# Kernel optimization log

Measured on AMD Instinct MI355X. Metric: run time of the kernel, lower is better.

## Reference

```python
import jax, jax.numpy as jnp
import numpy as np
import math

DIM = 768
EMB = 768          # dim * num_heads (num_heads=1)
NBLOCKS = 4
M = EMB // 2       # kernel_ratio = 0.5 -> 384 random features
EPS = 1e-8


def monarch_linear(x, w1, w2, b):
    """Monarch (blockdiag butterfly) linear: x [..., n] -> [..., out].
    w1: (k, q, p) with n = k*p ; w2: (l, s, r) with k*q = l*r ; out = l*s."""
    lead = x.shape[:-1]
    k, q, p = w1.shape
    l, s, r = w2.shape
    xf = x.reshape(-1, k, p)                              # (B, k, p)
    o1 = jnp.einsum('bkp,kqp->bkq', xf, w1)               # (B, k, q)
    o1 = o1.transpose(0, 2, 1).reshape(-1, l, r)          # permute then (B, l, r)
    o2 = jnp.einsum('blr,lsr->bls', o1, w2)               # (B, l, s)
    out = o2.transpose(0, 2, 1).reshape(*lead, s * l)     # (B, s, l) flattened
    return out + b


def prm_exp(x, w):
    """FAVOR+ positive random features. x: [b,t,d], w: [m,d]."""
    xd = 0.5 * jnp.sum(x * x, axis=-1, keepdims=True)     # [b,t,1]
    wtx = jnp.einsum('btd,md->btm', x, w)                 # [b,t,m]
    return jnp.exp(wtx - xd) / math.sqrt(M)


def _monarch_params(rng, n_in, n_out, nblocks):
    in_blk = n_in // nblocks
    out_blk = n_out // nblocks
    if n_in < n_out:
        w1 = rng.standard_normal((nblocks, in_blk, in_blk)).astype(np.float32)
        w2 = rng.standard_normal((nblocks, out_blk, in_blk)).astype(np.float32)
    else:
        w1 = rng.standard_normal((nblocks, out_blk, in_blk)).astype(np.float32)
        w2 = rng.standard_normal((nblocks, out_blk, out_blk)).astype(np.float32)
    scale = 1.0 / math.sqrt(n_in)
    b = rng.standard_normal((n_out,)).astype(np.float32) * scale
    return w1 * scale, w2 * scale, b


def setup_inputs() -> dict:
    key = jax.random.key(0)
    x = jax.random.normal(key, (8, 4096, DIM), dtype=jnp.float32)
    rng = np.random.default_rng(0)
    kqv_w1, kqv_w2, kqv_b = _monarch_params(rng, DIM, 3 * EMB, NBLOCKS)
    proj_w1, proj_w2, proj_b = _monarch_params(rng, EMB, EMB, NBLOCKS)
    # orthogonal random-feature matrix, rows orthonormal, scaled by sqrt(m)
    a = rng.standard_normal((EMB, M)).astype(np.float64)
    qmat, _ = np.linalg.qr(a)                             # (EMB, M), cols orthonormal
    w = (qmat.T * math.sqrt(M)).astype(np.float32)        # (M, EMB)
    return {
        'x': x,
        'kqv_w1': jnp.asarray(kqv_w1), 'kqv_w2': jnp.asarray(kqv_w2), 'kqv_b': jnp.asarray(kqv_b),
        'proj_w1': jnp.asarray(proj_w1), 'proj_w2': jnp.asarray(proj_w2), 'proj_b': jnp.asarray(proj_b),
        'w': jnp.asarray(w),
    }


def reference(x, kqv_w1, kqv_w2, kqv_b, proj_w1, proj_w2, proj_b, w):
    kqv = monarch_linear(x, kqv_w1, kqv_w2, kqv_b)        # [b,t,3*EMB]
    k, q, v = jnp.split(kqv, 3, axis=-1)                  # order k,q,v as in torch.split
    kp = prm_exp(k, w)                                    # [b,t,m]
    qp = prm_exp(q, w)                                    # [b,t,m]
    D = jnp.einsum('btm,bm->bt', qp, kp.sum(axis=1))[:, :, None]   # [b,t,1]
    kptv = jnp.einsum('btn,btm->bnm', v, kp)              # [b,EMB,m]
    y = jnp.einsum('btm,bnm->btn', qp, kptv) / (D + EPS)  # [b,t,EMB]
    return monarch_linear(y, proj_w1, proj_w2, proj_b)
```

## Files before the change

kernel.cpp:

```cpp
#include <hip/hip_runtime.h>


#define NTOK   32768
#define RSQRTM 0.05103103630798288f

typedef _Float16 f16;
typedef f16   f16x8 __attribute__((ext_vector_type(8)));
typedef f16   f16x4 __attribute__((ext_vector_type(4)));
typedef f16   f16x2 __attribute__((ext_vector_type(2)));
typedef short s16x8 __attribute__((ext_vector_type(8)));
typedef float f32x4 __attribute__((ext_vector_type(4)));

typedef const void __attribute__((address_space(1))) gv_t;
typedef void       __attribute__((address_space(3))) lv_t;
#define GLL16(g, l) __builtin_amdgcn_global_load_lds((gv_t*)(g), (lv_t*)(l), 16, 0, 0)

__device__ __forceinline__ float b2f(unsigned short u){
  union{unsigned int i; float f;} v; v.i = ((unsigned int)u)<<16; return v.f;
}
__device__ __forceinline__ unsigned short f2b(float f){
  union{float f; unsigned int i;} v; v.f = f;
  unsigned int x = v.i;
  x += 0x7fffu + ((x>>16)&1u);
  return (unsigned short)(x>>16);
}

template<typename T> struct MfmaOp;
template<> struct MfmaOp<f16> {
  typedef f16x8 frag;
  static __device__ __forceinline__ f32x4 run(frag a, frag b, f32x4 c){
    return __builtin_amdgcn_mfma_f32_16x16x32_f16(a, b, c, 0, 0, 0);
  }
};
template<> struct MfmaOp<short> {
  typedef s16x8 frag;
  static __device__ __forceinline__ f32x4 run(frag a, frag b, f32x4 c){
    return __builtin_amdgcn_mfma_f32_16x16x32_bf16(a, b, c, 0, 0, 0);
  }
};

__global__ void cvt16(const float4* __restrict__ src, f16* __restrict__ dst, int n4){
  const int i = blockIdx.x*256 + threadIdx.x;
  if (i >= n4) return;
  const float4 v = src[i];
  f16x4 h; h[0]=(f16)v.x; h[1]=(f16)v.y; h[2]=(f16)v.z; h[3]=(f16)v.w;
  *reinterpret_cast<f16x4*>(dst + 4*(long)i) = h;
}
__global__ void build_wkqvT(const float* __restrict__ w1, const float* __restrict__ w2,
                            f16* __restrict__ Wt){
  const int idx = blockIdx.x*256 + threadIdx.x;
  const int j = idx / 768, i = idx % 768;
  const int k = i / 192, p = i % 192;
  const int s = j >> 2,  l = j & 3;
  float acc = 0.f;
  #pragma unroll 4
  for(int u=0; u<48; ++u)
    acc += w1[(k*192 + l*48+u)*192 + p] * w2[(l*576+s)*192 + 4*u+k];
  Wt[idx] = (f16)acc;
}
__global__ void build_wprojT(const float* __restrict__ w1, const float* __restrict__ w2,
                             unsigned short* __restrict__ Wt){
  const int idx = blockIdx.x*256 + threadIdx.x;
  const int j = idx / 768, i = idx % 768;
  const int k = i / 192, p = i % 192;
  const int s = j >> 2,  l = j & 3;
  float acc = 0.f;
  #pragma unroll 4
  for(int u=0; u<48; ++u)
    acc += w1[(k*192 + l*48+u)*192 + p] * w2[(l*192+s)*192 + 4*u+k];
  Wt[idx] = f2b(acc);
}

template<typename T, int BM, int BN, int EPI>
__global__ __launch_bounds__(256)
void mgemm(const T* __restrict__ A, int lda, long aB,
           const T* __restrict__ Bt, int ldb, long bB,
           int K, void* __restrict__ out, int ldo, long outB,
           void* __restrict__ out2,
           const float* __restrict__ aux, long auxB){
  constexpr int MT = BM/32, NT = BN/32;
  constexpr int IA = BM/64, IB = BN/64;
  __shared__ T As[BM*32];
  __shared__ T Bs[BN*32];
  typedef typename MfmaOp<T>::frag frag_t;

  const int tid = threadIdx.x, lane = tid & 63, w = tid >> 6;
  const int wm = w >> 1, wn = w & 1;
  const int bz = blockIdx.z;
  const long m0 = (long)blockIdx.y * BM;
  const int  n0 = blockIdx.x * BN;
  const T* Ab = A  + (long)bz*aB;
  const T* Bb = Bt + (long)bz*bB;

  f32x4 acc[MT][NT];
  const f32x4 zero = {0.f, 0.f, 0.f, 0.f};
  #pragma unroll
  for(int i=0;i<MT;i++)
    #pragma unroll
    for(int j=0;j<NT;j++) acc[i][j] = zero;

  for (int k0 = 0; k0 < K; k0 += 32){
    __syncthreads();
    #pragma unroll
    for (int i = 0; i < IA; ++i){
      const int e = (w*IA + i)*64 + lane;
      const int m = e >> 2, j = e & 3;
      GLL16(Ab + (m0 + m)*lda + k0 + j*8, As + (size_t)(w*IA + i)*512);
    }
    #pragma unroll
    for (int i = 0; i < IB; ++i){
      const int e = (w*IB + i)*64 + lane;
      const int n = e >> 2, j = e & 3;
      GLL16(Bb + (long)(n0 + n)*ldb + k0 + j*8, Bs + (size_t)(w*IB + i)*512);
    }
    __syncthreads();

    frag_t a[MT], b[NT];
    #pragma unroll
    for (int mt=0; mt<MT; ++mt)
      a[mt] = *reinterpret_cast<const frag_t*>(
        &As[(wm*MT*16 + mt*16 + (lane&15))*32 + (lane>>4)*8]);
    #pragma unroll
    for (int nt=0; nt<NT; ++nt)
      b[nt] = *reinterpret_cast<const frag_t*>(
        &Bs[(wn*NT*16 + nt*16 + (lane&15))*32 + (lane>>4)*8]);
    #pragma unroll
    for (int mt=0; mt<MT; ++mt)
      #pragma unroll
      for (int nt=0; nt<NT; ++nt)
        acc[mt][nt] = MfmaOp<T>::run(a[mt], b[nt], acc[mt][nt]);
  }

  const int q = lane >> 4, ln = lane & 15;
  #pragma unroll
  for (int mt=0; mt<MT; ++mt){
    const long mbase = m0 + wm*MT*16 + mt*16 + q*4;
    float xv[4];
    if constexpr(EPI==1 || EPI==2){
      #pragma unroll
      for(int r=0;r<4;r++) xv[r] = aux[mbase + r];
    }
    if constexpr(EPI==4){
      #pragma unroll
      for(int r=0;r<4;r++) xv[r] = 1.f/(aux[bz*auxB + mbase + r] + 1e-8f);
    }
    #pragma unroll
    for (int nt=0; nt<NT; ++nt){
      const int n = n0 + wn*NT*16 + nt*16 + ln;
      const f32x4 c = acc[mt][nt];
      if constexpr(EPI==0){
        if (n0 < 1536){
          f16* KQ = (f16*)out;
          const float bv = aux[n];
          #pragma unroll
          for(int r=0;r<4;r++) KQ[(mbase+r)*1536 + n] = (f16)(c[r] + bv);
        } else {
          unsigned short* VT = (unsigned short*)out2;
          const float bv = aux[n];
          ushort4 v;
          v.x = f2b(c[0]+bv); v.y = f2b(c[1]+bv); v.z = f2b(c[2]+bv); v.w = f2b(c[3]+bv);
          *reinterpret_cast<ushort4*>(&VT[(long)(n-1536)*32768 + mbase]) = v;
        }
      } else if constexpr(EPI==1){
        unsigned short* o = (unsigned short*)out;
        ushort4 v;
        v.x = f2b(__expf(c[0]-xv[0])*RSQRTM);
        v.y = f2b(__expf(c[1]-xv[1])*RSQRTM);
        v.z = f2b(__expf(c[2]-xv[2])*RSQRTM);
        v.w = f2b(__expf(c[3]-xv[3])*RSQRTM);
        *reinterpret_cast<ushort4*>(&o[(long)n*ldo + mbase]) = v;
      } else if constexpr(EPI==2){
        unsigned short* o = (unsigned short*)out;
        #pragma unroll
        for(int r=0;r<4;r++)
          o[(mbase+r)*ldo + n] = f2b(__expf(c[r]-xv[r])*RSQRTM);
      } else if constexpr(EPI==3){
        unsigned short* o = (unsigned short*)out + (long)bz*outB;
        #pragma unroll
        for(int r=0;r<4;r++) o[(mbase+r)*ldo + n] = f2b(c[r]);
      } else if constexpr(EPI==4){
        unsigned short* o = (unsigned short*)out + (long)bz*outB;
        #pragma unroll
        for(int r=0;r<4;r++) o[(mbase+r)*ldo + n] = f2b(c[r]*xv[r]);
      } else {
        float* o = (float*)out;
        const float bv = aux[n];
        #pragma unroll
        for(int r=0;r<4;r++) o[(mbase+r)*ldo + n] = c[r] + bv;
      }
    }
  }
}

__global__ void xd_kernel(const f16* __restrict__ KQ, float* __restrict__ xd){
  const int t = blockIdx.x*4 + (threadIdx.x>>6);
  const int lane = threadIdx.x & 63;
  const f16* row = KQ + (long)t*1536;
  float sk=0.f, sq=0.f;
  #pragma unroll
  for(int j=0;j<6;j++){
    const f16x2 a = *reinterpret_cast<const f16x2*>(&row[lane*2 + j*128]);
    const f16x2 b = *reinterpret_cast<const f16x2*>(&row[768 + lane*2 + j*128]);
    const float a0=(float)a[0], a1=(float)a[1], b0=(float)b[0], b1=(float)b[1];
    sk += a0*a0 + a1*a1;  sq += b0*b0 + b1*b1;
  }
  for(int off=32; off; off>>=1){ sk += __shfl_down(sk,off); sq += __shfl_down(sq,off); }
  if(lane==0){ xd[t] = 0.5f*sk; xd[NTOK + t] = 0.5f*sq; }
}
__global__ void ksum_kernel(const unsigned short* __restrict__ kpT, float* __restrict__ ksum){
  const int lane = threadIdx.x & 63, w = threadIdx.x >> 6;
  const int id = blockIdx.x*4 + w;
  const int m = id % 384, b = id / 384;
  const unsigned short* base = kpT + (long)m*32768 + b*4096;
  float acc = 0.f;
  #pragma unroll
  for(int j=0;j<16;j++){
    const ushort4 v = *reinterpret_cast<const ushort4*>(&base[lane*4 + j*256]);
    acc += b2f(v.x)+b2f(v.y)+b2f(v.z)+b2f(v.w);
  }
  for(int off=32; off; off>>=1) acc += __shfl_down(acc,off);
  if(lane==0) ksum[id] = acc;
}
__global__ void d_kernel(const unsigned short* __restrict__ qp,
                         const float* __restrict__ ksum, float* __restrict__ Dv){
  const int t = blockIdx.x*4 + (threadIdx.x>>6);
  const int lane = threadIdx.x & 63;
  const int b = t >> 12;
  const unsigned short* row = qp + (long)t*384;
  const float* ks = ksum + b*384;
  float acc = 0.f;
  #pragma unroll
  for(int j=0;j<6;j++){ const int m = lane + 64*j; acc += b2f(row[m])*ks[m]; }
  for(int off=32; off; off>>=1) acc += __shfl_down(acc,off);
  if(lane==0) Dv[t] = acc;
}

extern "C" void kernel_launch(void* const* d_in, const int* in_sizes, int n_in,
                              void* d_out, int out_size, void* d_ws, size_t ws_size,
                              hipStream_t stream){
  const float* x       = (const float*)d_in[0];
  const float* kqv_w1  = (const float*)d_in[1];
  const float* kqv_w2  = (const float*)d_in[2];
  const float* kqv_b   = (const float*)d_in[3];
  const float* proj_w1 = (const float*)d_in[4];
  const float* proj_w2 = (const float*)d_in[5];
  const float* proj_b  = (const float*)d_in[6];
  const float* w       = (const float*)d_in[7];
  char* ws = (char*)d_ws;

  const size_t o_WkqvT  = 0;
  const size_t o_WprojT = 3538944;
  const size_t o_w16    = 4718592;
  const size_t o_x16    = 5308416;
  const size_t o_KQ     = 55640064;
  const size_t o_VT     = 156303360;
  const size_t o_xd     = 206635008;
  const size_t o_kpT    = 206897152;
  const size_t o_qp     = 232062976;
  const size_t o_ksum   = 257228800;
  const size_t o_kptv   = 257241088;
  const size_t o_Dv     = 261959680;
  const size_t o_Y      = 262090752;
  const size_t TOTAL    = 312422400;
  if (ws_size < TOTAL) return;

  f16*            WkqvT  = (f16*)(ws + o_WkqvT);
  short*          WprojT = (short*)(ws + o_WprojT);
  f16*            w16    = (f16*)(ws + o_w16);
  f16*            x16    = (f16*)(ws + o_x16);
  f16*            KQ     = (f16*)(ws + o_KQ);
  short*          VT     = (short*)(ws + o_VT);
  float*          xd     = (float*)(ws + o_xd);
  short*          kpT    = (short*)(ws + o_kpT);
  short*          qp     = (short*)(ws + o_qp);
  float*          ksum   = (float*)(ws + o_ksum);
  short*          kptv   = (short*)(ws + o_kptv);
  float*          Dv     = (float*)(ws + o_Dv);
  short*          Y      = (short*)(ws + o_Y);

  cvt16<<<24576, 256, 0, stream>>>((const float4*)x, x16, 6291456);
  cvt16<<<288,   256, 0, stream>>>((const float4*)w, w16, 73728);
  build_wkqvT <<<6912, 256, 0, stream>>>(kqv_w1, kqv_w2, WkqvT);
  build_wprojT<<<2304, 256, 0, stream>>>(proj_w1, proj_w2, (unsigned short*)WprojT);

  mgemm<f16,128,128,0><<<dim3(18,256,1), 256, 0, stream>>>(
      x16, 768, 0L, WkqvT, 768, 0L, 768, KQ, 1536, 0L, VT, kqv_b, 0L);
  xd_kernel<<<8192, 256, 0, stream>>>(KQ, xd);

  mgemm<f16,128,128,1><<<dim3(3,256,1), 256, 0, stream>>>(
      KQ, 1536, 0L, w16, 768, 0L, 768, kpT, 32768, 0L, nullptr, xd, 0L);
  mgemm<f16,128,128,2><<<dim3(3,256,1), 256, 0, stream>>>(
      KQ + 768, 1536, 0L, w16, 768, 0L, 768, qp, 384, 0L, nullptr, xd + NTOK, 0L);

  ksum_kernel<<<768, 256, 0, stream>>>((const unsigned short*)kpT, ksum);

  mgemm<short,64,64,3><<<dim3(6,12,8), 256, 0, stream>>>(
      VT, 32768, 4096L, kpT, 32768, 4096L, 4096, kptv, 384, 294912L, nullptr, nullptr, 0L);

  d_kernel<<<8192, 256, 0, stream>>>((const unsigned short*)qp, ksum, Dv);

  mgemm<short,128,128,4><<<dim3(6,32,8), 256, 0, stream>>>(
      qp, 384, 1572864L, kptv, 384, 294912L, 384, Y, 768, 3145728L, nullptr, Dv, 4096L);

  mgemm<short,128,128,5><<<dim3(6,256,1), 256, 0, stream>>>(
      Y, 768, 0L, WprojT, 768, 0L, 768, d_out, 768, 0L, nullptr, proj_b, 0L);
}
```

Measured before the change: 678.8 us.

## Fuse reductions into GEMM epilogues, deepen K tile with swizzled LDS, split-K kptv

Folds the xd, ksum and D reductions into the GEMM epilogues using shuffles and atomics, removing three standalone reduction kernels and their re-reads of KQ, kpT and qp. The GEMM K step doubles to 64 with an XOR-swizzled LDS layout to cut LDS bank conflicts and halve the barrier count. The kptv GEMM becomes a 4-way split-K with 128x128 tiles writing fp32 partials, followed by a reduce kernel, which raises parallelism for that long-K GEMM. This adds atomics, a memset, extra workspace and fp32 partial traffic, and LDS use per block doubles.

```diff
diff --git a/kernel.cpp b/kernel.cpp
--- a/kernel.cpp
+++ b/kernel.cpp
@@ -7,7 +7,6 @@
 typedef _Float16 f16;
 typedef f16   f16x8 __attribute__((ext_vector_type(8)));
 typedef f16   f16x4 __attribute__((ext_vector_type(4)));
-typedef f16   f16x2 __attribute__((ext_vector_type(2)));
 typedef short s16x8 __attribute__((ext_vector_type(8)));
 typedef float f32x4 __attribute__((ext_vector_type(4)));
 
@@ -70,27 +69,37 @@
     acc += w1[(k*192 + l*48+u)*192 + p] * w2[(l*192+s)*192 + 4*u+k];
   Wt[idx] = f2b(acc);
 }
-
-template<typename T, int BM, int BN, int EPI>
+__global__ void reduce_kptv(const float* __restrict__ p32, unsigned short* __restrict__ o){
+  const int idx = blockIdx.x*256 + threadIdx.x;
+  const int b = idx / 294912, i = idx % 294912;
+  const float* base = p32 + (long)b*4*294912 + i;
+  o[idx] = f2b(base[0] + base[294912] + base[2*294912] + base[3*294912]);
+}
+
+template<typename T, int BM, int BN, int EPI, int SPLIT>
 __global__ __launch_bounds__(256)
 void mgemm(const T* __restrict__ A, int lda, long aB,
            const T* __restrict__ Bt, int ldb, long bB,
            int K, void* __restrict__ out, int ldo, long outB,
            void* __restrict__ out2,
-           const float* __restrict__ aux, long auxB){
+           const float* __restrict__ aux, long auxB,
+           float* __restrict__ aux2){
   constexpr int MT = BM/32, NT = BN/32;
-  constexpr int IA = BM/64, IB = BN/64;
-  __shared__ T As[BM*32];
-  __shared__ T Bs[BN*32];
+  constexpr int IA = BM/32, IB = BN/32;
+  __shared__ T As[BM*64];
+  __shared__ T Bs[BN*64];
   typedef typename MfmaOp<T>::frag frag_t;
 
   const int tid = threadIdx.x, lane = tid & 63, w = tid >> 6;
   const int wm = w >> 1, wn = w & 1;
+  const int ln = lane & 15, q = lane >> 4;
   const int bz = blockIdx.z;
+  const int batch = bz / SPLIT;
+  const int kstart = (bz % SPLIT) * K;
   const long m0 = (long)blockIdx.y * BM;
   const int  n0 = blockIdx.x * BN;
-  const T* Ab = A  + (long)bz*aB;
-  const T* Bb = Bt + (long)bz*bB;
+  const T* Ab = A  + (long)batch*aB;
+  const T* Bb = Bt + (long)batch*bB;
 
   f32x4 acc[MT][NT];
   const f32x4 zero = {0.f, 0.f, 0.f, 0.f};
@@ -99,145 +108,183 @@
     #pragma unroll
     for(int j=0;j<NT;j++) acc[i][j] = zero;
 
-  for (int k0 = 0; k0 < K; k0 += 32){
+  for (int k0 = kstart; k0 < kstart + K; k0 += 64){
     __syncthreads();
     #pragma unroll
     for (int i = 0; i < IA; ++i){
       const int e = (w*IA + i)*64 + lane;
-      const int m = e >> 2, j = e & 3;
+      const int m = e >> 3, j = (e & 7) ^ (m & 7);
       GLL16(Ab + (m0 + m)*lda + k0 + j*8, As + (size_t)(w*IA + i)*512);
     }
     #pragma unroll
     for (int i = 0; i < IB; ++i){
       const int e = (w*IB + i)*64 + lane;
-      const int n = e >> 2, j = e & 3;
+      const int n = e >> 3, j = (e & 7) ^ (n & 7);
       GLL16(Bb + (long)(n0 + n)*ldb + k0 + j*8, Bs + (size_t)(w*IB + i)*512);
     }
     __syncthreads();
 
-    frag_t a[MT], b[NT];
-    #pragma unroll
-    for (int mt=0; mt<MT; ++mt)
-      a[mt] = *reinterpret_cast<const frag_t*>(
-        &As[(wm*MT*16 + mt*16 + (lane&15))*32 + (lane>>4)*8]);
-    #pragma unroll
-    for (int nt=0; nt<NT; ++nt)
-      b[nt] = *reinterpret_cast<const frag_t*>(
-        &Bs[(wn*NT*16 + nt*16 + (lane&15))*32 + (lane>>4)*8]);
-    #pragma unroll
-    for (int mt=0; mt<MT; ++mt)
-      #pragma unroll
-      for (int nt=0; nt<NT; ++nt)
-        acc[mt][nt] = MfmaOp<T>::run(a[mt], b[nt], acc[mt][nt]);
-  }
-
-  const int q = lane >> 4, ln = lane & 15;
-  #pragma unroll
-  for (int mt=0; mt<MT; ++mt){
-    const long mbase = m0 + wm*MT*16 + mt*16 + q*4;
-    float xv[4];
-    if constexpr(EPI==1 || EPI==2){
+    #pragma unroll
+    for (int kk = 0; kk < 2; ++kk){
+      frag_t a[MT], b[NT];
+      #pragma unroll
+      for (int mt=0; mt<MT; ++mt){
+        const int r = wm*MT*16 + mt*16 + ln;
+        a[mt] = *reinterpret_cast<const frag_t*>(&As[(r*8 + ((kk*4+q) ^ (r&7)))*8]);
+      }
+      #pragma unroll
+      for (int nt=0; nt<NT; ++nt){
+        const int r = wn*NT*16 + nt*16 + ln;
+        b[nt] = *reinterpret_cast<const frag_t*>(&Bs[(r*8 + ((kk*4+q) ^ (r&7)))*8]);
+      }
+      #pragma unroll
+      for (int mt=0; mt<MT; ++mt)
+        #pragma unroll
+        for (int nt=0; nt<NT; ++nt)
+          acc[mt][nt] = MfmaOp<T>::run(a[mt], b[nt], acc[mt][nt]);
+    }
+  }
+
+  if constexpr(EPI==1){
+    const int b = (int)(m0 >> 12);
+    float cs[NT];
+    #pragma unroll
+    for(int nt=0;nt<NT;nt++) cs[nt]=0.f;
+    #pragma unroll
+    for (int mt=0; mt<MT; ++mt){
+      const long mbase = m0 + wm*MT*16 + mt*16 + q*4;
+      float xv[4];
       #pragma unroll
       for(int r=0;r<4;r++) xv[r] = aux[mbase + r];
-    }
-    if constexpr(EPI==4){
-      #pragma unroll
-      for(int r=0;r<4;r++) xv[r] = 1.f/(aux[bz*auxB + mbase + r] + 1e-8f);
-    }
-    #pragma unroll
-    for (int nt=0; nt<NT; ++nt){
-      const int n = n0 + wn*NT*16 + nt*16 + ln;
-      const f32x4 c = acc[mt][nt];
-      if constexpr(EPI==0){
-        if (n0 < 1536){
-          f16* KQ = (f16*)out;
-          const float bv = aux[n];
-          #pragma unroll
-          for(int r=0;r<4;r++) KQ[(mbase+r)*1536 + n] = (f16)(c[r] + bv);
-        } else {
-          unsigned short* VT = (unsigned short*)out2;
-          const float bv = aux[n];
-          ushort4 v;
-          v.x = f2b(c[0]+bv); v.y = f2b(c[1]+bv); v.z = f2b(c[2]+bv); v.w = f2b(c[3]+bv);
-          *reinterpret_cast<ushort4*>(&VT[(long)(n-1536)*32768 + mbase]) = v;
-        }
-      } else if constexpr(EPI==1){
-        unsigned short* o = (unsigned short*)out;
+      #pragma unroll
+      for (int nt=0; nt<NT; ++nt){
+        const int n = n0 + wn*NT*16 + nt*16 + ln;
+        const f32x4 c = acc[mt][nt];
         ushort4 v;
         v.x = f2b(__expf(c[0]-xv[0])*RSQRTM);
         v.y = f2b(__expf(c[1]-xv[1])*RSQRTM);
         v.z = f2b(__expf(c[2]-xv[2])*RSQRTM);
         v.w = f2b(__expf(c[3]-xv[3])*RSQRTM);
-        *reinterpret_cast<ushort4*>(&o[(long)n*ldo + mbase]) = v;
-      } else if constexpr(EPI==2){
-        unsigned short* o = (unsigned short*)out;
+        *reinterpret_cast<ushort4*>(&((unsigned short*)out)[(long)n*ldo + mbase]) = v;
+        cs[nt] += b2f(v.x)+b2f(v.y)+b2f(v.z)+b2f(v.w);
+      }
+    }
+    #pragma unroll
+    for (int nt=0; nt<NT; ++nt){
+      cs[nt] += __shfl_xor(cs[nt], 16);
+      cs[nt] += __shfl_xor(cs[nt], 32);
+      if (lane < 16)
+        atomicAdd(&aux2[b*384 + n0 + wn*NT*16 + nt*16 + lane], cs[nt]);
+    }
+    return;
+  }
+
+  #pragma unroll
+  for (int mt=0; mt<MT; ++mt){
+    const long mbase = m0 + wm*MT*16 + mt*16 + q*4;
+    if constexpr(EPI==0){
+      const int nw = n0 + wn*NT*16;
+      const int part = nw / 768;
+      float p[4] = {0.f,0.f,0.f,0.f};
+      #pragma unroll
+      for (int nt=0; nt<NT; ++nt){
+        const int n = nw + nt*16 + ln;
+        const f32x4 c = acc[mt][nt];
+        const float bv = aux[n];
+        if (part < 2){
+          f16* KQ = (f16*)out;
+          #pragma unroll
+          for(int r=0;r<4;r++){
+            const f16 h = (f16)(c[r] + bv);
+            KQ[(mbase+r)*1536 + n] = h;
+            const float hf = (float)h;
+            p[r] += hf*hf;
+          }
+        } else {
+          unsigned short* VT = (unsigned short*)out2;
+          ushort4 v;
+          v.x = f2b(c[0]+bv); v.y = f2b(c[1]+bv); v.z = f2b(c[2]+bv); v.w = f2b(c[3]+bv);
+          *reinterpret_cast<ushort4*>(&VT[(long)(n-1536)*32768 + mbase]) = v;
+        }
+      }
+      if (part < 2){
+        #pragma unroll
+        for(int r=0;r<4;r++){
+          #pragma unroll
+          for(int mask=1; mask<16; mask<<=1) p[r] += __shfl_xor(p[r], mask);
+        }
+        if (ln == 0){
+          #pragma unroll
+          for(int r=0;r<4;r++)
+            atomicAdd(&aux2[part*NTOK + mbase + r], 0.5f*p[r]);
+        }
+      }
+    } else if constexpr(EPI==2){
+      const int b = (int)(m0 >> 12);
+      float xv[4], dp[4] = {0.f,0.f,0.f,0.f};
+      #pragma unroll
+      for(int r=0;r<4;r++) xv[r] = aux[mbase + r];
+      #pragma unroll
+      for (int nt=0; nt<NT; ++nt){
+        const int n = n0 + wn*NT*16 + nt*16 + ln;
+        const f32x4 c = acc[mt][nt];
+        const float ksn = aux2[b*384 + n];
+        #pragma unroll
+        for(int r=0;r<4;r++){
+          const unsigned short h = f2b(__expf(c[r]-xv[r])*RSQRTM);
+          ((unsigned short*)out)[(mbase+r)*ldo + n] = h;
+          dp[r] += b2f(h)*ksn;
+        }
+      }
+      #pragma unroll
+      for(int r=0;r<4;r++){
+        #pragma unroll
+        for(int mask=1; mask<16; mask<<=1) dp[r] += __shfl_xor(dp[r], mask);
+      }
+      if (ln == 0){
         #pragma unroll
         for(int r=0;r<4;r++)
-          o[(mbase+r)*ldo + n] = f2b(__expf(c[r]-xv[r])*RSQRTM);
-      } else if constexpr(EPI==3){
-        unsigned short* o = (unsigned short*)out + (long)bz*outB;
-        #pragma unroll
-        for(int r=0;r<4;r++) o[(mbase+r)*ldo + n] = f2b(c[r]);
-      } else if constexpr(EPI==4){
-        unsigned short* o = (unsigned short*)out + (long)bz*outB;
+          atomicAdd(&((float*)out2)[mbase + r], dp[r]);
+      }
+    } else if constexpr(EPI==3){
+      float* o = (float*)out + (long)bz*outB;
+      #pragma unroll
+      for (int nt=0; nt<NT; ++nt){
+        const int n = n0 + wn*NT*16 + nt*16 + ln;
+        const f32x4 c = acc[mt][nt];
+        #pragma unroll
+        for(int r=0;r<4;r++) o[(mbase+r)*ldo + n] = c[r];
+      }
+    } else if constexpr(EPI==4){
+      unsigned short* o = (unsigned short*)out + (long)bz*outB;
+      float xv[4];
+      #pragma unroll
+      for(int r=0;r<4;r++) xv[r] = 1.f/(aux[bz*auxB + mbase + r] + 1e-8f);
+      #pragma unroll
+      for (int nt=0; nt<NT; ++nt){
+        const int n = n0 + wn*NT*16 + nt*16 + ln;
+        const f32x4 c = acc[mt][nt];
         #pragma unroll
         for(int r=0;r<4;r++) o[(mbase+r)*ldo + n] = f2b(c[r]*xv[r]);
-      } else {
-        float* o = (float*)out;
+      }
+    } else if constexpr(EPI==5){
+      float* o = (float*)out;
+      #pragma unroll
+      for (int nt=0; nt<NT; ++nt){
+        const int n = n0 + wn*NT*16 + nt*16 + ln;
+        const f32x4 c = acc[mt][nt];
         const float bv = aux[n];
         #pragma unroll
         for(int r=0;r<4;r++) o[(mbase+r)*ldo + n] = c[r] + bv;
       }
     }
   }
-}
-
-__global__ void xd_kernel(const f16* __restrict__ KQ, float* __restrict__ xd){
-  const int t = blockIdx.x*4 + (threadIdx.x>>6);
-  const int lane = threadIdx.x & 63;
-  const f16* row = KQ + (long)t*1536;
-  float sk=0.f, sq=0.f;
-  #pragma unroll
-  for(int j=0;j<6;j++){
-    const f16x2 a = *reinterpret_cast<const f16x2*>(&row[lane*2 + j*128]);
-    const f16x2 b = *reinterpret_cast<const f16x2*>(&row[768 + lane*2 + j*128]);
-    const float a0=(float)a[0], a1=(float)a[1], b0=(float)b[0], b1=(float)b[1];
-    sk += a0*a0 + a1*a1;  sq += b0*b0 + b1*b1;
-  }
-  for(int off=32; off; off>>=1){ sk += __shfl_down(sk,off); sq += __shfl_down(sq,off); }
-  if(lane==0){ xd[t] = 0.5f*sk; xd[NTOK + t] = 0.5f*sq; }
-}
-__global__ void ksum_kernel(const unsigned short* __restrict__ kpT, float* __restrict__ ksum){
-  const int lane = threadIdx.x & 63, w = threadIdx.x >> 6;
-  const int id = blockIdx.x*4 + w;
-  const int m = id % 384, b = id / 384;
-  const unsigned short* base = kpT + (long)m*32768 + b*4096;
-  float acc = 0.f;
-  #pragma unroll
-  for(int j=0;j<16;j++){
-    const ushort4 v = *reinterpret_cast<const ushort4*>(&base[lane*4 + j*256]);
-    acc += b2f(v.x)+b2f(v.y)+b2f(v.z)+b2f(v.w);
-  }
-  for(int off=32; off; off>>=1) acc += __shfl_down(acc,off);
-  if(lane==0) ksum[id] = acc;
-}
-__global__ void d_kernel(const unsigned short* __restrict__ qp,
-                         const float* __restrict__ ksum, float* __restrict__ Dv){
-  const int t = blockIdx.x*4 + (threadIdx.x>>6);
-  const int lane = threadIdx.x & 63;
-  const int b = t >> 12;
-  const unsigned short* row = qp + (long)t*384;
-  const float* ks = ksum + b*384;
-  float acc = 0.f;
-  #pragma unroll
-  for(int j=0;j<6;j++){ const int m = lane + 64*j; acc += b2f(row[m])*ks[m]; }
-  for(int off=32; off; off>>=1) acc += __shfl_down(acc,off);
-  if(lane==0) Dv[t] = acc;
 }
 
 extern "C" void kernel_launch(void* const* d_in, const int* in_sizes, int n_in,
                               void* d_out, int out_size, void* d_ws, size_t ws_size,
                               hipStream_t stream){
+  (void)in_sizes; (void)n_in; (void)out_size;
   const float* x       = (const float*)d_in[0];
   const float* kqv_w1  = (const float*)d_in[1];
   const float* kqv_w2  = (const float*)d_in[2];
@@ -255,13 +302,14 @@
   const size_t o_KQ     = 55640064;
   const size_t o_VT     = 156303360;
   const size_t o_xd     = 206635008;
-  const size_t o_kpT    = 206897152;
-  const size_t o_qp     = 232062976;
-  const size_t o_ksum   = 257228800;
-  const size_t o_kptv   = 257241088;
-  const size_t o_Dv     = 261959680;
-  const size_t o_Y      = 262090752;
-  const size_t TOTAL    = 312422400;
+  const size_t o_ksum   = 206897152;
+  const size_t o_Dv     = 206909440;
+  const size_t o_kpT    = 207040512;
+  const size_t o_qp     = 232206336;
+  const size_t o_kptv32 = 257372160;
+  const size_t o_kptv   = 295120896;
+  const size_t o_Y      = 299839488;
+  const size_t TOTAL    = 350171136;
   if (ws_size < TOTAL) return;
 
   f16*            WkqvT  = (f16*)(ws + o_WkqvT);
@@ -271,37 +319,39 @@
   f16*            KQ     = (f16*)(ws + o_KQ);
   short*          VT     = (short*)(ws + o_VT);
   float*          xd     = (float*)(ws + o_xd);
+  float*          ksum   = (float*)(ws + o_ksum);
+  float*          Dv     = (float*)(ws + o_Dv);
   short*          kpT    = (short*)(ws + o_kpT);
   short*          qp     = (short*)(ws + o_qp);
-  float*          ksum   = (float*)(ws + o_ksum);
-  short*          kptv   = (short*)(ws + o_kptv);
-  float*          Dv     = (float*)(ws + o_Dv);
+  float*          kptv32 = (float*)(ws + o_kptv32);
+  unsigned short* kptv   = (unsigned short*)(ws + o_kptv);
   short*          Y      = (short*)(ws + o_Y);
+
+  hipMemsetAsync(ws + o_xd, 0, 405504, stream);
 
   cvt16<<<24576, 256, 0, stream>>>((const float4*)x, x16, 6291456);
   cvt16<<<288,   256, 0, stream>>>((const float4*)w, w16, 73728);
   build_wkqvT <<<6912, 256, 0, stream>>>(kqv_w1, kqv_w2, WkqvT);
   build_wprojT<<<2304, 256, 0, stream>>>(proj_w1, proj_w2, (unsigned short*)WprojT);
 
-  mgemm<f16,128,128,0><<<dim3(18,256,1), 256, 0, stream>>>(
-      x16, 768, 0L, WkqvT, 768, 0L, 768, KQ, 1536, 0L, VT, kqv_b, 0L);
-  xd_kernel<<<8192, 256, 0, stream>>>(KQ, xd);
-
-  mgemm<f16,128,128,1><<<dim3(3,256,1), 256, 0, stream>>>(
-      KQ, 1536, 0L, w16, 768, 0L, 768, kpT, 32768, 0L, nullptr, xd, 0L);
-  mgemm<f16,128,128,2><<<dim3(3,256,1), 256, 0, stream>>>(
-      KQ + 768, 1536, 0L, w16, 768, 0L, 768, qp, 384, 0L, nullptr, xd + NTOK, 0L);
-
-  ksum_kernel<<<768, 256, 0, stream>>>((const unsigned short*)kpT, ksum);
-
-  mgemm<short,64,64,3><<<dim3(6,12,8), 256, 0, stream>>>(
-      VT, 32768, 4096L, kpT, 32768, 4096L, 4096, kptv, 384, 294912L, nullptr, nullptr, 0L);
-
-  d_kernel<<<8192, 256, 0, stream>>>((const unsigned short*)qp, ksum, Dv);
-
-  mgemm<short,128,128,4><<<dim3(6,32,8), 256, 0, stream>>>(
-      qp, 384, 1572864L, kptv, 384, 294912L, 384, Y, 768, 3145728L, nullptr, Dv, 4096L);
-
-  mgemm<short,128,128,5><<<dim3(6,256,1), 256, 0, stream>>>(
-      Y, 768, 0L, WprojT, 768, 0L, 768, d_out, 768, 0L, nullptr, proj_b, 0L);
-}
+  mgemm<f16,128,128,0,1><<<dim3(18,256,1), 256, 0, stream>>>(
+      x16, 768, 0L, WkqvT, 768, 0L, 768, KQ, 1536, 0L, VT, kqv_b, 0L, xd);
+
+  mgemm<f16,128,128,1,1><<<dim3(3,256,1), 256, 0, stream>>>(
+      KQ, 1536, 0L, w16, 768, 0L, 768, kpT, 32768, 0L, nullptr, xd, 0L, ksum);
+
+  mgemm<f16,128,128,2,1><<<dim3(3,256,1), 256, 0, stream>>>(
+      KQ + 768, 1536, 0L, w16, 768, 0L, 768, qp, 384, 0L, Dv, xd + NTOK, 0L, ksum);
+
+  mgemm<short,128,128,3,4><<<dim3(3,6,32), 256, 0, stream>>>(
+      VT, 32768, 4096L, kpT, 32768, 4096L, 1024, kptv32, 384, 294912L,
+      nullptr, nullptr, 0L, nullptr);
+  reduce_kptv<<<9216, 256, 0, stream>>>(kptv32, kptv);
+
+  mgemm<short,128,128,4,1><<<dim3(6,32,8), 256, 0, stream>>>(
+      qp, 384, 1572864L, (short*)kptv, 384, 294912L, 384, Y, 768, 3145728L,
+      nullptr, Dv, 4096L, nullptr);
+
+  mgemm<short,128,128,5,1><<<dim3(6,256,1), 256, 0, stream>>>(
+      Y, 768, 0L, WprojT, 768, 0L, 768, d_out, 768, 0L, nullptr, proj_b, 0L, nullptr);
+}
```

Result: faster. 651.5 us (-4.0%).
